# Performance work log

Hardware: AMD Instinct MI355X
Metric: run time of the kernel (lower is better)

## Reference

```python
import jax, jax.numpy as jnp
import numpy as np

B, T, F, H, P = 4, 1024, 500, 128, 64


def setup_inputs() -> dict:
    key = jax.random.key(0)
    ks = jax.random.split(key, 10)
    s_gru = 1.0 / np.sqrt(H)
    s_ctx = 1.0 / np.sqrt(2 * H * P)
    s_fc = 1.0 / np.sqrt(H)
    return {
        "x": jax.random.normal(ks[0], (B, T, F), dtype=jnp.float32),
        "W_ih": jax.random.uniform(ks[1], (3 * H, F), jnp.float32, -s_gru, s_gru),
        "W_hh": jax.random.uniform(ks[2], (3 * H, H), jnp.float32, -s_gru, s_gru),
        "b_ih": jax.random.uniform(ks[3], (3 * H,), jnp.float32, -s_gru, s_gru),
        "b_hh": jax.random.uniform(ks[4], (3 * H,), jnp.float32, -s_gru, s_gru),
        "W_ctx": jax.random.uniform(ks[5], (H, 2 * H * P), jnp.float32, -s_ctx, s_ctx),
        "b_ctx": jax.random.uniform(ks[6], (H,), jnp.float32, -s_ctx, s_ctx),
        "W_fc": jax.random.uniform(ks[7], (P, H), jnp.float32, -s_fc, s_fc),
        "b_fc": jax.random.uniform(ks[8], (P,), jnp.float32, -s_fc, s_fc),
    }


def reference(x, W_ih, W_hh, b_ih, b_hh, W_ctx, b_ctx, W_fc, b_fc):
    # Original torch code never updates `hidden` inside the time loop, so every
    # GRU step runs with h = 0 (W_hh contributes only through b_hh). For a
    # 1-layer GRU, output == new state. PyTorch gate order: r, z, n.
    Bv, Tv, _ = x.shape
    Hv = W_hh.shape[1]
    Pv = W_fc.shape[0]
    gi = jnp.einsum('btf,gf->btg', x, W_ih) + b_ih          # [B,T,3H]
    gr, gz, gn = jnp.split(gi, 3, axis=-1)
    br, bz, bn = jnp.split(b_hh, 3)
    r = jax.nn.sigmoid(gr + br)
    z = jax.nn.sigmoid(gz + bz)
    n = jnp.tanh(gn + r * bn)                               # W_hh @ 0 == 0
    states = (1.0 - z) * n                                  # [B,T,H], h' = (1-z)*n + z*0
    all_states = jnp.transpose(states, (1, 0, 2))           # [T,B,H]

    # context_mat[:, :, j] at step i = concat(state_i, state_{max(i-j,0)})
    idx = jnp.clip(jnp.arange(Tv)[:, None] - jnp.arange(Pv)[None, :], 0)  # [T,P]
    gathered = all_states[idx]                              # [T,P,B,H]
    part1 = jnp.broadcast_to(all_states[:, :, :, None], (Tv, Bv, Hv, Pv))
    part2 = jnp.transpose(gathered, (0, 2, 3, 1))           # [T,B,H,P]
    # flatten matches torch .view(B, -1) of [B, 2H, P]: channel-major then proposal
    ctx_in = jnp.concatenate([part1, part2], axis=2).reshape(Tv, Bv, 2 * Hv * Pv)
    gate = jax.nn.sigmoid(jnp.einsum('tbc,hc->tbh', ctx_in, W_ctx) + b_ctx)
    gated = all_states * gate                               # output_i * ctx gate

    outs = jnp.transpose(gated, (1, 0, 2))                  # [B,T,H]
    probs = jax.nn.sigmoid(jnp.einsum('bth,ph->btp', outs, W_fc) + b_fc)
    probs = jnp.clip(probs, 0.001, 0.999)                   # [B,T,P]
    return probs, all_states
```

## Files before the change

kernel.cpp:

```cpp
#include <hip/hip_runtime.h>


typedef short bf16x8 __attribute__((ext_vector_type(8)));
typedef float f32x4 __attribute__((ext_vector_type(4)));
typedef float f32x16 __attribute__((ext_vector_type(16)));
typedef unsigned short u16;
typedef unsigned int u32;

__device__ __forceinline__ float bf2f(u16 u) {
  union { u32 i; float f; } v; v.i = ((u32)u) << 16; return v.f;
}
__device__ __forceinline__ u16 f2bf(float f) {
  union { float f; u32 i; } v; v.f = f;
  u32 u = v.i;
  return (u16)((u + 0x7FFFu + ((u >> 16) & 1u)) >> 16);
}
__device__ __forceinline__ u32 pack2(float a, float b) {
  return (u32)f2bf(a) | ((u32)f2bf(b) << 16);
}
__device__ __forceinline__ float sigmoidf_(float x) {
  return 1.0f / (1.0f + __expf(-x));
}

__global__ __launch_bounds__(256) void k_prep(const float* __restrict__ W_ctx,
                                              u16* __restrict__ WcT) {
  const int tid = threadIdx.x;
  __shared__ float t1[128][68];
  __shared__ float t2[128][68];
  __shared__ float s1[128];
  const int hp = blockIdx.x;
  const float* wrow = W_ctx + hp * 16384;
  for (int it = 0; it < 8; ++it) {
    int i = it * 256 + tid;
    int j = i * 4;
    int h = j >> 6, q = j & 63;
    *(float4*)&t1[h][q] = *(const float4*)(wrow + j);
    *(float4*)&t2[h][q] = *(const float4*)(wrow + 8192 + j);
  }
  __syncthreads();
  if (tid < 128) {
    float s = 0.f;
    for (int q = 0; q < 64; ++q) s += t1[tid][q];
    s1[tid] = s;
  }
  __syncthreads();
  for (int it = 0; it < 8; ++it) {
    int i = it * 256 + tid;
    int p = i >> 5, h0 = (i & 31) * 4;
    float v0 = t2[h0 + 0][p], v1 = t2[h0 + 1][p];
    float v2 = t2[h0 + 2][p], v3 = t2[h0 + 3][p];
    if (p == 0) { v0 += s1[h0]; v1 += s1[h0 + 1]; v2 += s1[h0 + 2]; v3 += s1[h0 + 3]; }
    uint2 o; o.x = pack2(v0, v1); o.y = pack2(v2, v3);
    *(uint2*)(WcT + ((size_t)(p * 16 + (h0 >> 3)) * 128 + hp) * 8 + (h0 & 7)) = o;
  }
}

__global__ __launch_bounds__(512, 4) void k_gemm_gi(const float* __restrict__ x,
                                                    const float* __restrict__ W_ih,
                                                    u16* __restrict__ gi_bf) {
  __shared__ u16 Asm[2][64][64];
  __shared__ u16 Bsm[2][128][64];
  const int tid = threadIdx.x;
  const int w = tid >> 6, lane = tid & 63;
  const int l15 = lane & 15, quad = lane >> 4;
  const int wm = (w & 1) * 32, wn = (w >> 1) * 32;
  const int m0 = blockIdx.x * 64;
  const int n0 = blockIdx.y * 128;
  f32x4 acc[2][2];
  for (int i = 0; i < 2; ++i)
    for (int j = 0; j < 2; ++j) acc[i][j] = (f32x4){0.f, 0.f, 0.f, 0.f};

  uint4 ra, rb[2];
  auto cvt_load = [](const float* base, int k) -> uint4 {
    float4 a = make_float4(0.f, 0.f, 0.f, 0.f), b = a;
    if (k < 500)     a = *(const float4*)(base + k);
    if (k + 4 < 500) b = *(const float4*)(base + k + 4);
    uint4 o; o.x = pack2(a.x, a.y); o.y = pack2(a.z, a.w);
    o.z = pack2(b.x, b.y); o.w = pack2(b.z, b.w);
    return o;
  };
  auto load_step = [&](int s) {
    int kc = s * 64;
    {
      int c = tid;
      ra = cvt_load(x + (size_t)(m0 + (c >> 3)) * 500, kc + (c & 7) * 8);
    }
#pragma unroll
    for (int j = 0; j < 2; ++j) {
      int c = j * 512 + tid;
      rb[j] = cvt_load(W_ih + (size_t)(n0 + (c >> 3)) * 500, kc + (c & 7) * 8);
    }
  };
  auto write_step = [&](int b) {
    {
      int c = tid;
      int r = c >> 3, pc = (c & 7) ^ (r & 7);
      *(uint4*)&Asm[b][r][pc * 8] = ra;
    }
#pragma unroll
    for (int j = 0; j < 2; ++j) {
      int c = j * 512 + tid;
      int r = c >> 3, pc = (c & 7) ^ (r & 7);
      *(uint4*)&Bsm[b][r][pc * 8] = rb[j];
    }
  };

  load_step(0); write_step(0); __syncthreads();
  for (int s = 0; s < 8; ++s) {
    int cur = s & 1;
    if (s < 7) load_step(s + 1);
#pragma unroll
    for (int kk = 0; kk < 2; ++kk) {
      int ch = kk * 4 + quad;
      bf16x8 af[2], bfr[2];
#pragma unroll
      for (int mt = 0; mt < 2; ++mt) {
        int r = wm + mt * 16 + l15;
        af[mt] = *(const bf16x8*)&Asm[cur][r][(ch ^ (r & 7)) * 8];
      }
#pragma unroll
      for (int nt = 0; nt < 2; ++nt) {
        int r = wn + nt * 16 + l15;
        bfr[nt] = *(const bf16x8*)&Bsm[cur][r][(ch ^ (r & 7)) * 8];
      }
#pragma unroll
      for (int mt = 0; mt < 2; ++mt)
#pragma unroll
        for (int nt = 0; nt < 2; ++nt)
          acc[mt][nt] = __builtin_amdgcn_mfma_f32_16x16x32_bf16(af[mt], bfr[nt], acc[mt][nt], 0, 0, 0);
    }
    if (s < 7) write_step((s + 1) & 1);
    __syncthreads();
  }
  for (int mt = 0; mt < 2; ++mt)
    for (int nt = 0; nt < 2; ++nt)
      for (int rg = 0; rg < 4; ++rg) {
        int m = m0 + wm + mt * 16 + quad * 4 + rg;
        int n = n0 + wn + nt * 16 + l15;
        gi_bf[m * 384 + n] = f2bf(acc[mt][nt][rg]);
      }
}

__global__ void k_states(const u16* __restrict__ gi_bf,
                         const float* __restrict__ b_ih, const float* __restrict__ b_hh,
                         u16* __restrict__ S_bf, float* __restrict__ out_states) {
  int g = blockIdx.x * 256 + threadIdx.x;
  int r = g >> 7, h = g & 127;
  float xr = bf2f(gi_bf[r * 384 + h])       + b_ih[h]       + b_hh[h];
  float xz = bf2f(gi_bf[r * 384 + 128 + h]) + b_ih[128 + h] + b_hh[128 + h];
  float xn = bf2f(gi_bf[r * 384 + 256 + h]) + b_ih[256 + h];
  float rg = sigmoidf_(xr);
  float zg = sigmoidf_(xz);
  float n = tanhf(xn + rg * b_hh[256 + h]);
  float s = (1.f - zg) * n;
  int b = r >> 10, t = r & 1023;
  S_bf[(t * 4 + b) * 128 + h] = f2bf(s);
  out_states[(t * 4 + b) * 128 + h] = s;
}

__global__ __launch_bounds__(256, 2) void k_gemm_ctx(const u16* __restrict__ S_bf,
                                                     const u16* __restrict__ WcT,
                                                     float* __restrict__ partial) {
  __shared__ u16 Awin[92][128];
  const int tid = threadIdx.x;
  const int w = tid >> 6, lane = tid & 63;
  const int l31 = lane & 31, half = lane >> 5;
  const int wm = (w & 1) * 32;
  const int wn = (w >> 1) * 64;
  const int m0 = blockIdx.x * 64;
  const int P0 = blockIdx.y * 8;
  const int tlo = (m0 >> 2) - P0 - 7;
  f32x16 acc[2];
#pragma unroll
  for (int i = 0; i < 16; ++i) { acc[0][i] = 0.f; acc[1][i] = 0.f; }

  for (int it = 0; it < 6; ++it) {
    int idx = it * 256 + tid;
    if (idx < 1472) {
      int r = idx >> 4, ch = idx & 15;
      int t = tlo + (r >> 2); if (t < 0) t = 0;
      uint4 v = *(const uint4*)(S_bf + (size_t)(t * 4 + (r & 3)) * 128 + ch * 8);
      *(uint4*)&Awin[r][((ch ^ (r & 15)) & 15) * 8] = v;
    }
  }
  __syncthreads();

  const u16* wbase = WcT + (size_t)half * 1024 + (size_t)(wn + l31) * 8;
#pragma unroll
  for (int pi = 0; pi < 8; ++pi) {
    const int shift = 4 * (7 - pi);
    const size_t pofs = (size_t)((P0 + pi) * 16) * 1024;
#pragma unroll
    for (int ks = 0; ks < 8; ++ks) {
      bf16x8 bfr[2];
#pragma unroll
      for (int nt = 0; nt < 2; ++nt)
        bfr[nt] = *(const bf16x8*)(wbase + pofs + (size_t)(ks * 2) * 1024 + nt * 256);
      int r = wm + shift + l31;
      int kc = ks * 2 + half;
      bf16x8 af = *(const bf16x8*)&Awin[r][((kc ^ (r & 15)) & 15) * 8];
#pragma unroll
      for (int nt = 0; nt < 2; ++nt)
        acc[nt] = __builtin_amdgcn_mfma_f32_32x32x16_bf16(af, bfr[nt], acc[nt], 0, 0, 0);
    }
  }
  float* op = partial + (size_t)blockIdx.y * 524288;
#pragma unroll
  for (int nt = 0; nt < 2; ++nt)
#pragma unroll
    for (int rg = 0; rg < 16; ++rg) {
      int m = m0 + wm + (rg & 3) + 8 * (rg >> 2) + 4 * half;
      int n = wn + nt * 32 + l31;
      op[m * 128 + n] = acc[nt][rg];
    }
}

__global__ __launch_bounds__(256) void k_epilogue(const float* __restrict__ partial,
                                                  const float* __restrict__ states,
                                                  const float* __restrict__ b_ctx,
                                                  const float* __restrict__ W_fc,
                                                  const float* __restrict__ b_fc,
                                                  float* __restrict__ out_probs) {
  __shared__ float Wfc2[64][128];
  __shared__ float gated[8][128];
  const int tid = threadIdx.x;
  const int row0 = blockIdx.x * 8;
  for (int it = 0; it < 8; ++it) {
    int i = it * 256 + tid;
    int pp = i >> 5, c = i & 31;
    float4 v = *(const float4*)(W_fc + i * 4);
    *(float4*)&Wfc2[pp][((c ^ pp) & 31) * 4] = v;
  }
  for (int it = 0; it < 4; ++it) {
    int i = it * 256 + tid;
    int lr = i >> 7, h = i & 127;
    int sr = row0 + lr;
    float gp = b_ctx[h];
#pragma unroll
    for (int c = 0; c < 8; ++c) gp += partial[(size_t)c * 524288 + sr * 128 + h];
    gated[lr][h] = states[sr * 128 + h] * sigmoidf_(gp);
  }
  __syncthreads();
  for (int it = 0; it < 2; ++it) {
    int o = it * 256 + tid;
    int lr = o >> 6, pp = o & 63;
    int sr = row0 + lr;
    float dot = 0.f;
#pragma unroll
    for (int i = 0; i < 32; ++i) {
      float4 g = *(const float4*)&gated[lr][i * 4];
      float4 wv = *(const float4*)&Wfc2[pp][((i ^ pp) & 31) * 4];
      dot += g.x * wv.x + g.y * wv.y + g.z * wv.z + g.w * wv.w;
    }
    float pv = sigmoidf_(dot + b_fc[pp]);
    pv = (pv > 0.001f) ? pv : 0.001f;
    pv = (pv < 0.999f) ? pv : 0.999f;
    int t = sr >> 2, b = sr & 3;
    out_probs[(b * 1024 + t) * 64 + pp] = pv;
  }
}

extern "C" void kernel_launch(void* const* d_in, const int* in_sizes, int n_in,
                              void* d_out, int out_size, void* d_ws, size_t ws_size,
                              hipStream_t stream) {
  const float* x     = (const float*)d_in[0];
  const float* W_ih  = (const float*)d_in[1];
  const float* b_ih  = (const float*)d_in[3];
  const float* b_hh  = (const float*)d_in[4];
  const float* W_ctx = (const float*)d_in[5];
  const float* b_ctx = (const float*)d_in[6];
  const float* W_fc  = (const float*)d_in[7];
  const float* b_fc  = (const float*)d_in[8];
  float* out = (float*)d_out;

  char* ws = (char*)d_ws;
  u16*   gi_bf   = (u16*)  (ws + 0);
  u16*   S_bf    = (u16*)  (ws + 3145728);
  u16*   WcT     = (u16*)  (ws + 4194304);
  float* partial = (float*)(ws + 6291456);

  k_prep<<<128, 256, 0, stream>>>(W_ctx, WcT);
  k_gemm_gi<<<dim3(64, 3), 512, 0, stream>>>(x, W_ih, gi_bf);
  k_states<<<2048, 256, 0, stream>>>(gi_bf, b_ih, b_hh, S_bf, out + 262144);
  k_gemm_ctx<<<dim3(64, 8), 256, 0, stream>>>(S_bf, WcT, partial);
  k_epilogue<<<512, 256, 0, stream>>>(partial, out + 262144, b_ctx, W_fc, b_fc, out);
}
```

Measured before the change: 124.4 us.

## Merge prep and input GEMM kernels, vectorize states, retile ctx GEMM, widen epilogue

Fuses the W_ctx repack and the input-projection GEMM into one launch, assigning them to disjoint block ranges so the two independent jobs run concurrently and one launch is removed. The prep path now row-sums W_ctx with wave shuffles instead of staging the first half in shared memory. The states kernel handles four hidden units per thread with vector loads and stores. The context GEMM drops to two waves per block, each covering two M tiles, so B fragments are reused across tiles. The epilogue processes 16 rows per block with float4 partial reads. The cost is lower ctx GEMM occupancy and higher register pressure.

```diff
diff --git a/kernel.cpp b/kernel.cpp
--- a/kernel.cpp
+++ b/kernel.cpp
@@ -22,160 +22,190 @@
   return 1.0f / (1.0f + __expf(-x));
 }
 
-__global__ __launch_bounds__(256) void k_prep(const float* __restrict__ W_ctx,
-                                              u16* __restrict__ WcT) {
+__global__ __launch_bounds__(512, 4) void k_front(const float* __restrict__ x,
+                                                  const float* __restrict__ W_ih,
+                                                  u16* __restrict__ gi_bf,
+                                                  const float* __restrict__ W_ctx,
+                                                  u16* __restrict__ WcT) {
+  __shared__ __align__(16) char smem[49152];
   const int tid = threadIdx.x;
-  __shared__ float t1[128][68];
-  __shared__ float t2[128][68];
-  __shared__ float s1[128];
-  const int hp = blockIdx.x;
-  const float* wrow = W_ctx + hp * 16384;
-  for (int it = 0; it < 8; ++it) {
-    int i = it * 256 + tid;
-    int j = i * 4;
-    int h = j >> 6, q = j & 63;
-    *(float4*)&t1[h][q] = *(const float4*)(wrow + j);
-    *(float4*)&t2[h][q] = *(const float4*)(wrow + 8192 + j);
-  }
-  __syncthreads();
-  if (tid < 128) {
-    float s = 0.f;
-    for (int q = 0; q < 64; ++q) s += t1[tid][q];
-    s1[tid] = s;
-  }
-  __syncthreads();
-  for (int it = 0; it < 8; ++it) {
-    int i = it * 256 + tid;
-    int p = i >> 5, h0 = (i & 31) * 4;
-    float v0 = t2[h0 + 0][p], v1 = t2[h0 + 1][p];
-    float v2 = t2[h0 + 2][p], v3 = t2[h0 + 3][p];
-    if (p == 0) { v0 += s1[h0]; v1 += s1[h0 + 1]; v2 += s1[h0 + 2]; v3 += s1[h0 + 3]; }
-    uint2 o; o.x = pack2(v0, v1); o.y = pack2(v2, v3);
-    *(uint2*)(WcT + ((size_t)(p * 16 + (h0 >> 3)) * 128 + hp) * 8 + (h0 & 7)) = o;
-  }
-}
-
-__global__ __launch_bounds__(512, 4) void k_gemm_gi(const float* __restrict__ x,
-                                                    const float* __restrict__ W_ih,
-                                                    u16* __restrict__ gi_bf) {
-  __shared__ u16 Asm[2][64][64];
-  __shared__ u16 Bsm[2][128][64];
-  const int tid = threadIdx.x;
-  const int w = tid >> 6, lane = tid & 63;
-  const int l15 = lane & 15, quad = lane >> 4;
-  const int wm = (w & 1) * 32, wn = (w >> 1) * 32;
-  const int m0 = blockIdx.x * 64;
-  const int n0 = blockIdx.y * 128;
-  f32x4 acc[2][2];
-  for (int i = 0; i < 2; ++i)
-    for (int j = 0; j < 2; ++j) acc[i][j] = (f32x4){0.f, 0.f, 0.f, 0.f};
-
-  uint4 ra, rb[2];
-  auto cvt_load = [](const float* base, int k) -> uint4 {
-    float4 a = make_float4(0.f, 0.f, 0.f, 0.f), b = a;
-    if (k < 500)     a = *(const float4*)(base + k);
-    if (k + 4 < 500) b = *(const float4*)(base + k + 4);
-    uint4 o; o.x = pack2(a.x, a.y); o.y = pack2(a.z, a.w);
-    o.z = pack2(b.x, b.y); o.w = pack2(b.z, b.w);
-    return o;
-  };
-  auto load_step = [&](int s) {
-    int kc = s * 64;
+  const int bid = blockIdx.x;
+
+  if (bid < 192) {
+    typedef u16 AsmT[64][64];
+    typedef u16 BsmT[128][64];
+    AsmT* Asm = (AsmT*)smem;
+    BsmT* Bsm = (BsmT*)(smem + 16384);
+    const int w = tid >> 6, lane = tid & 63;
+    const int l15 = lane & 15, quad = lane >> 4;
+    const int wm = (w & 1) * 32, wn = (w >> 1) * 32;
+    const int m0 = (bid & 63) * 64;
+    const int n0 = (bid >> 6) * 128;
+    f32x4 acc[2][2];
+    for (int i = 0; i < 2; ++i)
+      for (int j = 0; j < 2; ++j) acc[i][j] = (f32x4){0.f, 0.f, 0.f, 0.f};
+
+    uint4 ra, rb[2];
+    auto cvt_load = [](const float* base, int k) -> uint4 {
+      float4 a = make_float4(0.f, 0.f, 0.f, 0.f), b = a;
+      if (k < 500)     a = *(const float4*)(base + k);
+      if (k + 4 < 500) b = *(const float4*)(base + k + 4);
+      uint4 o; o.x = pack2(a.x, a.y); o.y = pack2(a.z, a.w);
+      o.z = pack2(b.x, b.y); o.w = pack2(b.z, b.w);
+      return o;
+    };
+    auto load_step = [&](int s) {
+      int kc = s * 64;
+      {
+        int c = tid;
+        ra = cvt_load(x + (size_t)(m0 + (c >> 3)) * 500, kc + (c & 7) * 8);
+      }
+#pragma unroll
+      for (int j = 0; j < 2; ++j) {
+        int c = j * 512 + tid;
+        rb[j] = cvt_load(W_ih + (size_t)(n0 + (c >> 3)) * 500, kc + (c & 7) * 8);
+      }
+    };
+    auto write_step = [&](int b) {
+      {
+        int c = tid;
+        int r = c >> 3, pc = (c & 7) ^ (r & 7);
+        *(uint4*)&Asm[b][r][pc * 8] = ra;
+      }
+#pragma unroll
+      for (int j = 0; j < 2; ++j) {
+        int c = j * 512 + tid;
+        int r = c >> 3, pc = (c & 7) ^ (r & 7);
+        *(uint4*)&Bsm[b][r][pc * 8] = rb[j];
+      }
+    };
+
+    load_step(0); write_step(0); __syncthreads();
+    for (int s = 0; s < 8; ++s) {
+      int cur = s & 1;
+      if (s < 7) load_step(s + 1);
+#pragma unroll
+      for (int kk = 0; kk < 2; ++kk) {
+        int ch = kk * 4 + quad;
+        bf16x8 af[2], bfr[2];
+#pragma unroll
+        for (int mt = 0; mt < 2; ++mt) {
+          int r = wm + mt * 16 + l15;
+          af[mt] = *(const bf16x8*)&Asm[cur][r][(ch ^ (r & 7)) * 8];
+        }
+#pragma unroll
+        for (int nt = 0; nt < 2; ++nt) {
+          int r = wn + nt * 16 + l15;
+          bfr[nt] = *(const bf16x8*)&Bsm[cur][r][(ch ^ (r & 7)) * 8];
+        }
+#pragma unroll
+        for (int mt = 0; mt < 2; ++mt)
+#pragma unroll
+          for (int nt = 0; nt < 2; ++nt)
+            acc[mt][nt] = __builtin_amdgcn_mfma_f32_16x16x32_bf16(af[mt], bfr[nt], acc[mt][nt], 0, 0, 0);
+      }
+      if (s < 7) write_step((s + 1) & 1);
+      __syncthreads();
+    }
+    for (int mt = 0; mt < 2; ++mt)
+      for (int nt = 0; nt < 2; ++nt)
+        for (int rg = 0; rg < 4; ++rg) {
+          int m = m0 + wm + mt * 16 + quad * 4 + rg;
+          int n = n0 + wn + nt * 16 + l15;
+          gi_bf[m * 384 + n] = f2bf(acc[mt][nt][rg]);
+        }
+  } else {
+    typedef float T2Row[68];
+    T2Row* t2 = (T2Row*)smem;
+    float* s1 = (float*)(smem + 34816);
+    const int hp = bid - 192;
+    const float* wrow = W_ctx + hp * 16384;
+    for (int it = 0; it < 4; ++it) {
+      int i = it * 512 + tid;
+      int j = i * 4;
+      int h = j >> 6, q = j & 63;
+      *(float4*)&t2[h][q] = *(const float4*)(wrow + 8192 + j);
+    }
     {
-      int c = tid;
-      ra = cvt_load(x + (size_t)(m0 + (c >> 3)) * 500, kc + (c & 7) * 8);
-    }
-#pragma unroll
-    for (int j = 0; j < 2; ++j) {
-      int c = j * 512 + tid;
-      rb[j] = cvt_load(W_ih + (size_t)(n0 + (c >> 3)) * 500, kc + (c & 7) * 8);
-    }
-  };
-  auto write_step = [&](int b) {
-    {
-      int c = tid;
-      int r = c >> 3, pc = (c & 7) ^ (r & 7);
-      *(uint4*)&Asm[b][r][pc * 8] = ra;
-    }
-#pragma unroll
-    for (int j = 0; j < 2; ++j) {
-      int c = j * 512 + tid;
-      int r = c >> 3, pc = (c & 7) ^ (r & 7);
-      *(uint4*)&Bsm[b][r][pc * 8] = rb[j];
-    }
-  };
-
-  load_step(0); write_step(0); __syncthreads();
-  for (int s = 0; s < 8; ++s) {
-    int cur = s & 1;
-    if (s < 7) load_step(s + 1);
-#pragma unroll
-    for (int kk = 0; kk < 2; ++kk) {
-      int ch = kk * 4 + quad;
-      bf16x8 af[2], bfr[2];
-#pragma unroll
-      for (int mt = 0; mt < 2; ++mt) {
-        int r = wm + mt * 16 + l15;
-        af[mt] = *(const bf16x8*)&Asm[cur][r][(ch ^ (r & 7)) * 8];
-      }
-#pragma unroll
-      for (int nt = 0; nt < 2; ++nt) {
-        int r = wn + nt * 16 + l15;
-        bfr[nt] = *(const bf16x8*)&Bsm[cur][r][(ch ^ (r & 7)) * 8];
-      }
-#pragma unroll
-      for (int mt = 0; mt < 2; ++mt)
-#pragma unroll
-        for (int nt = 0; nt < 2; ++nt)
-          acc[mt][nt] = __builtin_amdgcn_mfma_f32_16x16x32_bf16(af[mt], bfr[nt], acc[mt][nt], 0, 0, 0);
-    }
-    if (s < 7) write_step((s + 1) & 1);
+      const int w = tid >> 6, lane = tid & 63;
+      for (int rr = w; rr < 128; rr += 8) {
+        float v = wrow[rr * 64 + lane];
+#pragma unroll
+        for (int off = 32; off; off >>= 1) v += __shfl_down(v, off, 64);
+        if (lane == 0) s1[rr] = v;
+      }
+    }
     __syncthreads();
-  }
-  for (int mt = 0; mt < 2; ++mt)
-    for (int nt = 0; nt < 2; ++nt)
-      for (int rg = 0; rg < 4; ++rg) {
-        int m = m0 + wm + mt * 16 + quad * 4 + rg;
-        int n = n0 + wn + nt * 16 + l15;
-        gi_bf[m * 384 + n] = f2bf(acc[mt][nt][rg]);
-      }
+    for (int it = 0; it < 4; ++it) {
+      int i = it * 512 + tid;
+      int p = i >> 5, h0 = (i & 31) * 4;
+      float v0 = t2[h0 + 0][p], v1 = t2[h0 + 1][p];
+      float v2 = t2[h0 + 2][p], v3 = t2[h0 + 3][p];
+      if (p == 0) { v0 += s1[h0]; v1 += s1[h0 + 1]; v2 += s1[h0 + 2]; v3 += s1[h0 + 3]; }
+      uint2 o; o.x = pack2(v0, v1); o.y = pack2(v2, v3);
+      *(uint2*)(WcT + ((size_t)(p * 16 + (h0 >> 3)) * 128 + hp) * 8 + (h0 & 7)) = o;
+    }
+  }
 }
 
 __global__ void k_states(const u16* __restrict__ gi_bf,
                          const float* __restrict__ b_ih, const float* __restrict__ b_hh,
                          u16* __restrict__ S_bf, float* __restrict__ out_states) {
   int g = blockIdx.x * 256 + threadIdx.x;
-  int r = g >> 7, h = g & 127;
-  float xr = bf2f(gi_bf[r * 384 + h])       + b_ih[h]       + b_hh[h];
-  float xz = bf2f(gi_bf[r * 384 + 128 + h]) + b_ih[128 + h] + b_hh[128 + h];
-  float xn = bf2f(gi_bf[r * 384 + 256 + h]) + b_ih[256 + h];
-  float rg = sigmoidf_(xr);
-  float zg = sigmoidf_(xz);
-  float n = tanhf(xn + rg * b_hh[256 + h]);
-  float s = (1.f - zg) * n;
+  int r = g >> 5, h0 = (g & 31) * 4;
+  const u16* gr = gi_bf + r * 384;
+  uint2 ur = *(const uint2*)(gr + h0);
+  uint2 uz = *(const uint2*)(gr + 128 + h0);
+  uint2 un = *(const uint2*)(gr + 256 + h0);
+  float4 bir = *(const float4*)(b_ih + h0);
+  float4 biz = *(const float4*)(b_ih + 128 + h0);
+  float4 bin = *(const float4*)(b_ih + 256 + h0);
+  float4 bhr = *(const float4*)(b_hh + h0);
+  float4 bhz = *(const float4*)(b_hh + 128 + h0);
+  float4 bhn = *(const float4*)(b_hh + 256 + h0);
+  float xr[4] = { bf2f((u16)ur.x) + bir.x + bhr.x, bf2f((u16)(ur.x >> 16)) + bir.y + bhr.y,
+                  bf2f((u16)ur.y) + bir.z + bhr.z, bf2f((u16)(ur.y >> 16)) + bir.w + bhr.w };
+  float xz[4] = { bf2f((u16)uz.x) + biz.x + bhz.x, bf2f((u16)(uz.x >> 16)) + biz.y + bhz.y,
+                  bf2f((u16)uz.y) + biz.z + bhz.z, bf2f((u16)(uz.y >> 16)) + biz.w + bhz.w };
+  float xn[4] = { bf2f((u16)un.x) + bin.x, bf2f((u16)(un.x >> 16)) + bin.y,
+                  bf2f((u16)un.y) + bin.z, bf2f((u16)(un.y >> 16)) + bin.w };
+  float bn[4] = { bhn.x, bhn.y, bhn.z, bhn.w };
+  float s[4];
+#pragma unroll
+  for (int j = 0; j < 4; ++j) {
+    float rg = sigmoidf_(xr[j]);
+    float zg = sigmoidf_(xz[j]);
+    float n = tanhf(xn[j] + rg * bn[j]);
+    s[j] = (1.f - zg) * n;
+  }
   int b = r >> 10, t = r & 1023;
-  S_bf[(t * 4 + b) * 128 + h] = f2bf(s);
-  out_states[(t * 4 + b) * 128 + h] = s;
-}
-
-__global__ __launch_bounds__(256, 2) void k_gemm_ctx(const u16* __restrict__ S_bf,
+  size_t o = (size_t)(t * 4 + b) * 128 + h0;
+  uint2 sb; sb.x = pack2(s[0], s[1]); sb.y = pack2(s[2], s[3]);
+  *(uint2*)(S_bf + o) = sb;
+  float4 so = make_float4(s[0], s[1], s[2], s[3]);
+  *(float4*)(out_states + o) = so;
+}
+
+__global__ __launch_bounds__(128, 2) void k_gemm_ctx(const u16* __restrict__ S_bf,
                                                      const u16* __restrict__ WcT,
                                                      float* __restrict__ partial) {
   __shared__ u16 Awin[92][128];
   const int tid = threadIdx.x;
   const int w = tid >> 6, lane = tid & 63;
   const int l31 = lane & 31, half = lane >> 5;
-  const int wm = (w & 1) * 32;
-  const int wn = (w >> 1) * 64;
+  const int wn = w * 64;
   const int m0 = blockIdx.x * 64;
   const int P0 = blockIdx.y * 8;
   const int tlo = (m0 >> 2) - P0 - 7;
-  f32x16 acc[2];
-#pragma unroll
-  for (int i = 0; i < 16; ++i) { acc[0][i] = 0.f; acc[1][i] = 0.f; }
-
-  for (int it = 0; it < 6; ++it) {
-    int idx = it * 256 + tid;
+  f32x16 acc[2][2];
+#pragma unroll
+  for (int i = 0; i < 16; ++i) {
+    acc[0][0][i] = 0.f; acc[0][1][i] = 0.f;
+    acc[1][0][i] = 0.f; acc[1][1][i] = 0.f;
+  }
+
+  for (int it = 0; it < 12; ++it) {
+    int idx = it * 128 + tid;
     if (idx < 1472) {
       int r = idx >> 4, ch = idx & 15;
       int t = tlo + (r >> 2); if (t < 0) t = 0;
@@ -189,30 +219,37 @@
 #pragma unroll
   for (int pi = 0; pi < 8; ++pi) {
     const int shift = 4 * (7 - pi);
-    const size_t pofs = (size_t)((P0 + pi) * 16) * 1024;
+    const u16* wp = wbase + (size_t)((P0 + pi) * 16) * 1024;
 #pragma unroll
     for (int ks = 0; ks < 8; ++ks) {
       bf16x8 bfr[2];
-#pragma unroll
-      for (int nt = 0; nt < 2; ++nt)
-        bfr[nt] = *(const bf16x8*)(wbase + pofs + (size_t)(ks * 2) * 1024 + nt * 256);
-      int r = wm + shift + l31;
+      bfr[0] = *(const bf16x8*)(wp + (size_t)(ks * 2) * 1024);
+      bfr[1] = *(const bf16x8*)(wp + (size_t)(ks * 2) * 1024 + 256);
       int kc = ks * 2 + half;
-      bf16x8 af = *(const bf16x8*)&Awin[r][((kc ^ (r & 15)) & 15) * 8];
-#pragma unroll
-      for (int nt = 0; nt < 2; ++nt)
-        acc[nt] = __builtin_amdgcn_mfma_f32_32x32x16_bf16(af, bfr[nt], acc[nt], 0, 0, 0);
+      bf16x8 af[2];
+#pragma unroll
+      for (int mt = 0; mt < 2; ++mt) {
+        int r = mt * 32 + shift + l31;
+        af[mt] = *(const bf16x8*)&Awin[r][((kc ^ (r & 15)) & 15) * 8];
+      }
+#pragma unroll
+      for (int mt = 0; mt < 2; ++mt)
+#pragma unroll
+        for (int nt = 0; nt < 2; ++nt)
+          acc[mt][nt] = __builtin_amdgcn_mfma_f32_32x32x16_bf16(af[mt], bfr[nt], acc[mt][nt], 0, 0, 0);
     }
   }
   float* op = partial + (size_t)blockIdx.y * 524288;
 #pragma unroll
-  for (int nt = 0; nt < 2; ++nt)
-#pragma unroll
-    for (int rg = 0; rg < 16; ++rg) {
-      int m = m0 + wm + (rg & 3) + 8 * (rg >> 2) + 4 * half;
-      int n = wn + nt * 32 + l31;
-      op[m * 128 + n] = acc[nt][rg];
-    }
+  for (int mt = 0; mt < 2; ++mt)
+#pragma unroll
+    for (int nt = 0; nt < 2; ++nt)
+#pragma unroll
+      for (int rg = 0; rg < 16; ++rg) {
+        int m = m0 + mt * 32 + (rg & 3) + 8 * (rg >> 2) + 4 * half;
+        int n = wn + nt * 32 + l31;
+        op[m * 128 + n] = acc[mt][nt][rg];
+      }
 }
 
 __global__ __launch_bounds__(256) void k_epilogue(const float* __restrict__ partial,
@@ -222,26 +259,35 @@
                                                   const float* __restrict__ b_fc,
                                                   float* __restrict__ out_probs) {
   __shared__ float Wfc2[64][128];
-  __shared__ float gated[8][128];
+  __shared__ float gated[16][128];
   const int tid = threadIdx.x;
-  const int row0 = blockIdx.x * 8;
+  const int row0 = blockIdx.x * 16;
   for (int it = 0; it < 8; ++it) {
     int i = it * 256 + tid;
     int pp = i >> 5, c = i & 31;
     float4 v = *(const float4*)(W_fc + i * 4);
     *(float4*)&Wfc2[pp][((c ^ pp) & 31) * 4] = v;
   }
+  for (int it = 0; it < 2; ++it) {
+    int i = it * 256 + tid;
+    int lr = i >> 5, h0 = (i & 31) * 4;
+    int sr = row0 + lr;
+    float4 gp = *(const float4*)(b_ctx + h0);
+#pragma unroll
+    for (int c = 0; c < 8; ++c) {
+      float4 pv = *(const float4*)(partial + (size_t)c * 524288 + (size_t)sr * 128 + h0);
+      gp.x += pv.x; gp.y += pv.y; gp.z += pv.z; gp.w += pv.w;
+    }
+    float4 st = *(const float4*)(states + (size_t)sr * 128 + h0);
+    float4 gv;
+    gv.x = st.x * sigmoidf_(gp.x);
+    gv.y = st.y * sigmoidf_(gp.y);
+    gv.z = st.z * sigmoidf_(gp.z);
+    gv.w = st.w * sigmoidf_(gp.w);
+    *(float4*)&gated[lr][h0] = gv;
+  }
+  __syncthreads();
   for (int it = 0; it < 4; ++it) {
-    int i = it * 256 + tid;
-    int lr = i >> 7, h = i & 127;
-    int sr = row0 + lr;
-    float gp = b_ctx[h];
-#pragma unroll
-    for (int c = 0; c < 8; ++c) gp += partial[(size_t)c * 524288 + sr * 128 + h];
-    gated[lr][h] = states[sr * 128 + h] * sigmoidf_(gp);
-  }
-  __syncthreads();
-  for (int it = 0; it < 2; ++it) {
     int o = it * 256 + tid;
     int lr = o >> 6, pp = o & 63;
     int sr = row0 + lr;
@@ -279,9 +325,8 @@
   u16*   WcT     = (u16*)  (ws + 4194304);
   float* partial = (float*)(ws + 6291456);
 
-  k_prep<<<128, 256, 0, stream>>>(W_ctx, WcT);
-  k_gemm_gi<<<dim3(64, 3), 512, 0, stream>>>(x, W_ih, gi_bf);
-  k_states<<<2048, 256, 0, stream>>>(gi_bf, b_ih, b_hh, S_bf, out + 262144);
-  k_gemm_ctx<<<dim3(64, 8), 256, 0, stream>>>(S_bf, WcT, partial);
-  k_epilogue<<<512, 256, 0, stream>>>(partial, out + 262144, b_ctx, W_fc, b_fc, out);
-}
+  k_front<<<320, 512, 0, stream>>>(x, W_ih, gi_bf, W_ctx, WcT);
+  k_states<<<512, 256, 0, stream>>>(gi_bf, b_ih, b_hh, S_bf, out + 262144);
+  k_gemm_ctx<<<dim3(64, 8), 128, 0, stream>>>(S_bf, WcT, partial);
+  k_epilogue<<<256, 256, 0, stream>>>(partial, out + 262144, b_ctx, W_fc, b_fc, out);
+}
```

Measured after the change: 129.6 us. 1.04x slower.
